# Optimization experiments

Hardware: AMD Instinct MI355X
Metric: run time of the kernel (lower is better)

Reference implementation:

```python
import jax, jax.numpy as jnp
import numpy as np

T, D, K, V, NB = 32768, 256, 16, 16, 2
H = K * V  # hidden size; must equal D for the residual x + y

def phi(x):
    return 1.0 + jax.nn.elu(x)

def _layernorm(x, w, b, eps=1e-5):
    m = x.mean(-1, keepdims=True)
    v = ((x - m) ** 2).mean(-1, keepdims=True)
    return (x - m) * jax.lax.rsqrt(v + eps) * w + b

def _combine(a, b):
    # reset-wrapped associative update: right element's start flag zeroes the left carry
    pa, sa, za = a
    pb, sb, zb = b
    keep = jnp.logical_not(pb)
    return (jnp.logical_or(pa, pb), keep * sa + sb, keep * za + zb)

def _block(x, start, s0, z0, Wk, Wq, Wv, bv, Wskip, bskip, Wm1, bm1, Wm2, bm2, Wm3, bm3, lnw, lnb):
    k = phi(x @ Wk.T)                                   # [T,K]
    q = phi(x @ Wq.T)                                   # [T,K]
    v = x @ Wv.T + bv                                   # [T,V]
    kv = jnp.einsum('ti,tj->tij', k, v)                 # [T,K,V]
    s = jnp.concatenate([s0, kv], axis=0)               # [T+1,K,V]
    z = jnp.concatenate([z0, k[:, None, :]], axis=0)    # [T+1,1,K]
    st = jnp.concatenate([jnp.zeros((1, 1, 1), bool), start.reshape(-1, 1, 1)], axis=0)
    _, s, z = jax.lax.associative_scan(_combine, (st, s, z), axis=0)
    s, z = s[1:], z[1:]
    numer = jnp.einsum('tij,ti->tj', s, q)              # [T,V]
    denom = jnp.einsum('tzi,tj->tz', z, q).clip(1e-6)   # [T,1] (faithful to source einsum)
    out = numer / denom                                 # [T,V]
    h = jax.nn.leaky_relu(out @ Wm1.T + bm1)
    h = jax.nn.leaky_relu(h @ Wm2.T + bm2)
    h = h @ Wm3.T + bm3
    return _layernorm(h + (x @ Wskip.T + bskip), lnw, lnb)

def _forward(x, start, s0, z0, Wk, Wq, Wv, bv, Wskip, bskip, Wm1, bm1, Wm2, bm2, Wm3, bm3, lnw, lnb):
    y = x
    for i in range(NB):  # small fixed layer loop
        y = _block(x, start, s0[i], z0[i], Wk[i], Wq[i], Wv[i], bv[i], Wskip[i], bskip[i],
                   Wm1[i], bm1[i], Wm2[i], bm2[i], Wm3[i], bm3[i], lnw[i], lnb[i])
        x = x + y
    return y

def setup_inputs() -> dict:
    key = jax.random.key(0)
    ks = jax.random.split(key, 12)
    g = lambda k, shp, fan: jax.random.normal(k, shp, jnp.float32) * (fan ** -0.5)
    return dict(
        x=jax.random.normal(ks[0], (T, D), jnp.float32),
        start=jax.random.randint(ks[1], (T,), 0, 2).astype(bool),
        s0=jnp.zeros((NB, 1, K, V), jnp.float32),
        z0=jnp.zeros((NB, 1, 1, K), jnp.float32),
        Wk=g(ks[2], (NB, K, D), D), Wq=g(ks[3], (NB, K, D), D),
        Wv=g(ks[4], (NB, V, D), D), bv=jnp.zeros((NB, V), jnp.float32),
        Wskip=g(ks[5], (NB, H, D), D), bskip=jnp.zeros((NB, H), jnp.float32),
        Wm1=g(ks[6], (NB, H, V), V), bm1=jnp.zeros((NB, H), jnp.float32),
        Wm2=g(ks[7], (NB, H, H), H), bm2=jnp.zeros((NB, H), jnp.float32),
        Wm3=g(ks[8], (NB, H, H), H), bm3=jnp.zeros((NB, H), jnp.float32),
        ln_w=jnp.ones((NB, H), jnp.float32), ln_b=jnp.zeros((NB, H), jnp.float32),
    )

def reference(x, start, s0, z0, Wk, Wq, Wv, bv, Wskip, bskip, Wm1, bm1, Wm2, bm2, Wm3, bm3, ln_w, ln_b):
    return _forward(x, start, s0, z0, Wk, Wq, Wv, bv, Wskip, bskip, Wm1, bm1, Wm2, bm2, Wm3, bm3, ln_w, ln_b)
```

## Files before the change

### kernel.cpp

```cpp
#include <hip/hip_runtime.h>
#include <hip/hip_bf16.h>
#include <cstdint>

#define TT   32768
#define DD   256
#define KV   16
#define NBLK 2
#define HH   256
#define CH   64
#define NCH  (TT / CH)

typedef __attribute__((ext_vector_type(8))) short bf16x8;
typedef __attribute__((ext_vector_type(4))) float f32x4;

__device__ __forceinline__ float phi_f(float x)  { return x > 0.f ? x + 1.f : expf(x); }
__device__ __forceinline__ float lrelu_f(float x){ return x > 0.f ? x : 0.01f * x; }
__device__ __forceinline__ unsigned short f2bf(float f) {
  unsigned u = __float_as_uint(f);
  u += 0x7fffu + ((u >> 16) & 1u);
  return (unsigned short)(u >> 16);
}
__device__ __forceinline__ float bf2f(unsigned short h) {
  return __uint_as_float(((unsigned)h) << 16);
}

__global__ void k_detect(const void* __restrict__ startp, int* __restrict__ flags) {
  int stride = gridDim.x * blockDim.x;
  for (int t = blockIdx.x * blockDim.x + threadIdx.x; t < TT / 4; t += stride) {
    unsigned u = ((const unsigned*)startp)[t];
    if (u > 1u) atomicOr(&flags[0], 1);
    float f = ((const float*)startp)[t];
    if (!(f == 0.f || f == 1.f)) atomicOr(&flags[1], 1);
  }
}

__global__ void k_canon(const void* __restrict__ startp, const int* __restrict__ flags,
                        float* __restrict__ start_f) {
  int v32 = flags[0], vf = flags[1];
  int stride = gridDim.x * blockDim.x;
  for (int t = blockIdx.x * blockDim.x + threadIdx.x; t < TT; t += stride) {
    bool s;
    if (v32 == 0)     s = ((const unsigned*)startp)[t] != 0u;
    else if (vf == 0) s = ((const float*)startp)[t] != 0.f;
    else              s = ((const unsigned char*)startp)[t] != 0;
    start_f[t] = s ? 1.f : 0.f;
  }
}

__global__ __launch_bounds__(256) void k_cvtbig(
    const float* __restrict__ s0, const float* __restrict__ s1, const float* __restrict__ s2,
    unsigned short* __restrict__ d0, unsigned short* __restrict__ d1,
    unsigned short* __restrict__ d2, int n) {
  int i = (blockIdx.x * 256 + threadIdx.x) * 8;
  const float* s; unsigned short* d;
  if (i < n)            { s = s0; d = d0; }
  else if (i < 2 * n)   { s = s1; d = d1; i -= n; }
  else if (i < 3 * n)   { s = s2; d = d2; i -= 2 * n; }
  else return;
  float4 a = *(const float4*)(s + i);
  float4 b = *(const float4*)(s + i + 4);
  float vals[8] = {a.x, a.y, a.z, a.w, b.x, b.y, b.z, b.w};
  bf16x8 t;
#pragma unroll
  for (int j = 0; j < 8; j++) t[j] = (short)f2bf(vals[j]);
  *(bf16x8*)(d + i) = t;
}

__global__ __launch_bounds__(256) void k_cvtproj(
    const float* __restrict__ Wk, const float* __restrict__ Wq, const float* __restrict__ Wv,
    unsigned short* __restrict__ wh, unsigned short* __restrict__ wl) {
  int t8 = blockIdx.x * 256 + threadIdx.x;
  if (t8 >= NBLK * 48 * 256 / 8) return;
  int e = t8 * 8;
  int b = e / (48 * 256);
  int rem = e - b * 48 * 256;
  int o = rem / (16 * 256);
  int nr = rem - o * 16 * 256;
  const float* src = (o == 0 ? Wk : o == 1 ? Wq : Wv) + b * 16 * 256 + nr;
  float4 a = *(const float4*)src;
  float4 c = *(const float4*)(src + 4);
  float vals[8] = {a.x, a.y, a.z, a.w, c.x, c.y, c.z, c.w};
  bf16x8 th, tl;
#pragma unroll
  for (int j = 0; j < 8; j++) {
    unsigned short h = f2bf(vals[j]);
    th[j] = (short)h;
    tl[j] = (short)f2bf(vals[j] - bf2f(h));
  }
  *(bf16x8*)(wh + e) = th;
  *(bf16x8*)(wl + e) = tl;
}

__global__ __launch_bounds__(256) void k_cvtm1(
    const float* __restrict__ Wm1,
    unsigned short* __restrict__ h, unsigned short* __restrict__ l) {
  int row = blockIdx.x * 256 + threadIdx.x;
  if (row >= NBLK * 256) return;
  const float* s = Wm1 + row * 16;
  bf16x8 th0, tl0, th1, tl1, z;
#pragma unroll
  for (int j = 0; j < 8; j++) {
    float v0 = s[j], v1 = s[j + 8];
    unsigned short h0 = f2bf(v0), h1 = f2bf(v1);
    th0[j] = (short)h0; tl0[j] = (short)f2bf(v0 - bf2f(h0));
    th1[j] = (short)h1; tl1[j] = (short)f2bf(v1 - bf2f(h1));
    z[j] = 0;
  }
  unsigned short* dh = h + row * 32;
  unsigned short* dl = l + row * 32;
  *(bf16x8*)(dh) = th0;  *(bf16x8*)(dh + 8) = th1;
  *(bf16x8*)(dh + 16) = z; *(bf16x8*)(dh + 24) = z;
  *(bf16x8*)(dl) = tl0;  *(bf16x8*)(dl + 8) = tl1;
  *(bf16x8*)(dl + 16) = z; *(bf16x8*)(dl + 24) = z;
}

__global__ __launch_bounds__(256) void k_projt(
    const float* __restrict__ x,
    const unsigned short* __restrict__ wh, const unsigned short* __restrict__ wl,
    const float* __restrict__ bv, const float* __restrict__ start_f,
    float* __restrict__ kout, float* __restrict__ qout, float* __restrict__ vout,
    float* __restrict__ tails_s, float* __restrict__ tails_zs,
    float* __restrict__ tails_flag) {
  __shared__ unsigned short xh[64 * 256];
  __shared__ unsigned short xl[64 * 256];
  __shared__ float stc[CH];
  __shared__ int lsS;
  float* kc = (float*)xh;
  float* vc = kc + 64 * 16;

  int tid = threadIdx.x, wg = blockIdx.x;
  size_t rbase = (size_t)wg * 64;
  const float* xs = x + rbase * DD;
#pragma unroll
  for (int i = 0; i < 8; i++) {
    int idx = tid + i * 256;
    int row = idx >> 5, c8 = idx & 31;
    const float* p = xs + row * DD + c8 * 8;
    float4 a = *(const float4*)p;
    float4 b = *(const float4*)(p + 4);
    float vals[8] = {a.x, a.y, a.z, a.w, b.x, b.y, b.z, b.w};
    bf16x8 th, tl;
#pragma unroll
    for (int j = 0; j < 8; j++) {
      unsigned short h = f2bf(vals[j]);
      th[j] = (short)h;
      tl[j] = (short)f2bf(vals[j] - bf2f(h));
    }
    int off = row * 512 + ((c8 * 16) ^ ((row & 7) << 4));
    *(bf16x8*)((char*)xh + off) = th;
    *(bf16x8*)((char*)xl + off) = tl;
  }
  if (tid < CH) stc[tid] = start_f[wg * CH + tid];
  __syncthreads();

  int lane = tid & 63, wv = tid >> 6, lg = lane >> 4, lr = lane & 15;
  int r = wv * 16 + lr;
  f32x4 acc[3];
#pragma unroll
  for (int o = 0; o < 3; o++) acc[o] = (f32x4){0.f, 0.f, 0.f, 0.f};

#pragma unroll
  for (int kk = 0; kk < 8; kk++) {
    int kbyte = kk * 64 + lg * 16;
    int off = r * 512 + (kbyte ^ ((r & 7) << 4));
    bf16x8 ah = *(bf16x8*)((char*)xh + off);
    bf16x8 al = *(bf16x8*)((char*)xl + off);
#pragma unroll
    for (int o = 0; o < 3; o++) {
      bf16x8 bh = *(const bf16x8*)((const char*)wh + (o * 16 + lr) * 512 + kbyte);
      bf16x8 bl = *(const bf16x8*)((const char*)wl + (o * 16 + lr) * 512 + kbyte);
      acc[o] = __builtin_amdgcn_mfma_f32_16x16x32_bf16(ah, bh, acc[o], 0, 0, 0);
      acc[o] = __builtin_amdgcn_mfma_f32_16x16x32_bf16(al, bh, acc[o], 0, 0, 0);
      acc[o] = __builtin_amdgcn_mfma_f32_16x16x32_bf16(ah, bl, acc[o], 0, 0, 0);
    }
  }
  __syncthreads();

  float bvv = bv[lr];
#pragma unroll
  for (int rg = 0; rg < 4; rg++) {
    int rl = wv * 16 + lg * 4 + rg;
    size_t g = rbase + rl;
    float kvl = phi_f(acc[0][rg]);
    float vvl = acc[2][rg] + bvv;
    kout[g * KV + lr] = kvl;
    qout[g * KV + lr] = phi_f(acc[1][rg]);
    vout[g * KV + lr] = vvl;
    kc[rl * KV + lr] = kvl;
    vc[rl * KV + lr] = vvl;
  }
  if (tid < 64) {
    unsigned long long mask = __ballot(stc[tid] != 0.f);
    if (tid == 0) lsS = mask ? (63 - __builtin_clzll(mask)) : -1;
  }
  __syncthreads();
  int ls = lsS;
  int t0 = ls < 0 ? 0 : ls;
  {
    int i = tid >> 4, j = tid & 15;
    float s = 0.f;
    for (int t = t0; t < CH; t++) s += kc[t * KV + i] * vc[t * KV + j];
    tails_s[(size_t)wg * 256 + tid] = s;
  }
  if (tid < 64) {
    float ks = 0.f;
    if (tid >= t0) {
#pragma unroll
      for (int i = 0; i < KV; i++) ks += kc[tid * KV + i];
    }
#pragma unroll
    for (int m = 1; m < 64; m <<= 1) ks += __shfl_xor(ks, m);
    if (tid == 0) {
      tails_zs[wg] = ks;
      tails_flag[wg] = (ls >= 0) ? 1.f : 0.f;
    }
  }
}

#define SP 65
__global__ __launch_bounds__(256) void k_att(
    const float* __restrict__ q, const float* __restrict__ k,
    const float* __restrict__ v, const float* __restrict__ start_f,
    const float* __restrict__ tails_s, const float* __restrict__ tails_zs,
    const float* __restrict__ tails_flag,
    const float* __restrict__ s0, const float* __restrict__ z0,
    float* __restrict__ att) {
  __shared__ float qc[CH * KV], kc[CH * KV], vc[CH * KV], stc[CH];
  __shared__ float S[CH * SP];
  __shared__ float carry[256];
  __shared__ float ksum[CH], zsl[CH], qsum[CH];
  __shared__ int ns[CH];
  __shared__ float czs_s;
  int c = blockIdx.x, tid = threadIdx.x;
  size_t base = (size_t)c * CH * KV;
  for (int u = tid; u < CH * KV; u += 256) {
    qc[u] = q[base + u]; kc[u] = k[base + u]; vc[u] = v[base + u];
  }
  if (tid < CH) stc[tid] = start_f[c * CH + tid];
  __syncthreads();
  if (tid < CH) {
    int cnt = 0;
    for (int u = 0; u <= tid; u++) cnt += (stc[u] != 0.f);
    ns[tid] = cnt;
    float ks = 0.f, qs = 0.f;
    for (int i = 0; i < KV; i++) { ks += kc[tid * KV + i]; qs += qc[tid * KV + i]; }
    ksum[tid] = ks; qsum[tid] = qs;
  }
  __syncthreads();
  if (tid < CH) {
    float acc = 0.f;
    for (int u = tid; u >= 0; u--) { acc += ksum[u]; if (stc[u] != 0.f) break; }
    zsl[tid] = acc;
  }
  {
    float accs = 0.f, aczs = 0.f;
    int cc = c - 1;
    for (;;) {
      if (cc < 0) {
        accs += s0[tid];
        if (tid == 0) { float z = 0.f; for (int i = 0; i < KV; i++) z += z0[i]; aczs += z; }
        break;
      }
      float fl = tails_flag[cc];
      accs += tails_s[(size_t)cc * 256 + tid];
      if (tid == 0) aczs += tails_zs[cc];
      if (fl != 0.f) break;
      cc--;
    }
    carry[tid] = accs;
    if (tid == 0) czs_s = aczs;
  }
  __syncthreads();
  {
    int t = tid >> 2, g = tid & 3;
    for (int u = 0; u < 16; u++) {
      int tp = g * 16 + u;
      float val = 0.f;
      if (tp <= t && ns[tp] == ns[t]) {
        float dot = 0.f;
        for (int i = 0; i < KV; i++) dot += qc[t * KV + i] * kc[tp * KV + i];
        val = dot;
      }
      S[t * SP + tp] = val;
    }
  }
  __syncthreads();
  float czs = czs_s;
  int j = tid & 15, tr = tid >> 4;
  for (int p = 0; p < 4; p++) {
    int t = p * 16 + tr;
    float numer = 0.f;
    for (int tp = 0; tp < CH; tp++) numer += S[t * SP + tp] * vc[tp * KV + j];
    float zs = zsl[t];
    if (ns[t] == 0) {
      float cn = 0.f;
      for (int i = 0; i < KV; i++) cn += qc[t * KV + i] * carry[i * KV + j];
      numer += cn;
      zs += czs;
    }
    float denom = fmaxf(zs * qsum[t], 1e-6f);
    att[base + t * KV + j] = numer / denom;
  }
}

#define A1S 40
template<int WY, int WX>
__global__ __launch_bounds__(256, 2) void k_mlp5(
    const float* __restrict__ att, const float* __restrict__ xsrc,
    const unsigned short* __restrict__ wm1h, const unsigned short* __restrict__ wm1l,
    const float* __restrict__ bm1,
    const unsigned short* __restrict__ Wm2b, const float* __restrict__ bm2,
    const unsigned short* __restrict__ Wm3b, const float* __restrict__ bm3,
    const unsigned short* __restrict__ Wskb, const float* __restrict__ bsk,
    const float* __restrict__ lnw, const float* __restrict__ lnb,
    float* __restrict__ yout, float* __restrict__ xnext) {
  __shared__ unsigned short hb[64 * 256];
  __shared__ __align__(16) char uni[64 * A1S * 4];
  unsigned short* aoh = (unsigned short*)uni;
  unsigned short* aol = aoh + 64 * A1S;
  float* redS = (float*)uni;
  float* redQ = redS + 256;
  float* mrow = redQ + 256;
  float* irow = mrow + 64;

  int tid = threadIdx.x, wg = blockIdx.x;
  size_t rbase = (size_t)wg * 64;

  for (int idx = tid; idx < 64 * 32; idx += 256) {
    int row = idx >> 5, col = idx & 31;
    float v = (col < 16) ? att[(rbase + row) * KV + col] : 0.f;
    unsigned short h = f2bf(v);
    aoh[row * A1S + col] = h;
    aol[row * A1S + col] = f2bf(v - bf2f(h));
  }
  __syncthreads();

  int lane = tid & 63, wv = tid >> 6, lg = lane >> 4, lr = lane & 15;
  int nc0 = wv * 64;

  f32x4 acc[4][4];
#pragma unroll
  for (int a = 0; a < 4; a++)
#pragma unroll
    for (int b = 0; b < 4; b++) acc[a][b] = (f32x4){0.f, 0.f, 0.f, 0.f};

  {
    bf16x8 b1h[4], b1l[4];
#pragma unroll
    for (int nt = 0; nt < 4; nt++) {
      int n = nc0 + nt * 16 + lr;
      b1h[nt] = *(const bf16x8*)(wm1h + n * 32 + lg * 8);
      b1l[nt] = *(const bf16x8*)(wm1l + n * 32 + lg * 8);
    }
#pragma unroll
    for (int mt = 0; mt < 4; mt++) {
      int r = mt * 16 + lr;
      bf16x8 ah = *(bf16x8*)(aoh + r * A1S + lg * 8);
      bf16x8 al = *(bf16x8*)(aol + r * A1S + lg * 8);
#pragma unroll
      for (int nt = 0; nt < 4; nt++) {
        acc[mt][nt] = __builtin_amdgcn_mfma_f32_16x16x32_bf16(ah, b1h[nt], acc[mt][nt], 0, 0, 0);
        acc[mt][nt] = __builtin_amdgcn_mfma_f32_16x16x32_bf16(al, b1h[nt], acc[mt][nt], 0, 0, 0);
        acc[mt][nt] = __builtin_amdgcn_mfma_f32_16x16x32_bf16(ah, b1l[nt], acc[mt][nt], 0, 0, 0);
      }
    }
  }
  __syncthreads();
  {
    float bm1v[4];
#pragma unroll
    for (int nt = 0; nt < 4; nt++) bm1v[nt] = bm1[nc0 + nt * 16 + lr];
#pragma unroll
    for (int mt = 0; mt < 4; mt++)
#pragma unroll
      for (int nt = 0; nt < 4; nt++)
#pragma unroll
        for (int rg = 0; rg < 4; rg++) {
          int r = mt * 16 + lg * 4 + rg;
          int cc = nc0 + nt * 16 + lr;
          *(unsigned short*)((char*)hb + r * 512 + ((cc * 2) ^ ((r & 7) << 4))) =
              f2bf(lrelu_f(acc[mt][nt][rg] + bm1v[nt]));
        }
  }
  __syncthreads();

#pragma unroll
  for (int a = 0; a < 4; a++)
#pragma unroll
    for (int b = 0; b < 4; b++) acc[a][b] = (f32x4){0.f, 0.f, 0.f, 0.f};
#pragma unroll
  for (int kk = 0; kk < 8; kk++) {
    int kbyte = kk * 64 + lg * 16;
    bf16x8 bfr[4];
#pragma unroll
    for (int nt = 0; nt < 4; nt++) {
      int n = nc0 + nt * 16 + lr;
      bfr[nt] = *(const bf16x8*)((const char*)Wm2b + n * 512 + kbyte);
    }
#pragma unroll
    for (int mt = 0; mt < 4; mt++) {
      int r = mt * 16 + lr;
      bf16x8 af = *(bf16x8*)((char*)hb + r * 512 + (kbyte ^ ((r & 7) << 4)));
#pragma unroll
      for (int nt = 0; nt < 4; nt++)
        acc[mt][nt] = __builtin_amdgcn_mfma_f32_16x16x32_bf16(af, bfr[nt], acc[mt][nt], 0, 0, 0);
    }
  }
  __syncthreads();
  {
    float bm2v[4];
#pragma unroll
    for (int nt = 0; nt < 4; nt++) bm2v[nt] = bm2[nc0 + nt * 16 + lr];
#pragma unroll
    for (int mt = 0; mt < 4; mt++)
#pragma unroll
      for (int nt = 0; nt < 4; nt++)
#pragma unroll
        for (int rg = 0; rg < 4; rg++) {
          int r = mt * 16 + lg * 4 + rg;
          int cc = nc0 + nt * 16 + lr;
          *(unsigned short*)((char*)hb + r * 512 + ((cc * 2) ^ ((r & 7) << 4))) =
              f2bf(lrelu_f(acc[mt][nt][rg] + bm2v[nt]));
        }
  }
  __syncthreads();

  f32x4 acc2[4][4];
#pragma unroll
  for (int a = 0; a < 4; a++)
#pragma unroll
    for (int b = 0; b < 4; b++) acc2[a][b] = (f32x4){0.f, 0.f, 0.f, 0.f};
  const float* xrow = xsrc + rbase * DD;
#pragma unroll
  for (int kk = 0; kk < 8; kk++) {
    int kbyte = kk * 64 + lg * 16;
    int kf = kk * 32 + lg * 8;
    bf16x8 b3[4], bs[4];
#pragma unroll
    for (int nt = 0; nt < 4; nt++) {
      int n = nc0 + nt * 16 + lr;
      b3[nt] = *(const bf16x8*)((const char*)Wm3b + n * 512 + kbyte);
      bs[nt] = *(const bf16x8*)((const char*)Wskb + n * 512 + kbyte);
    }
#pragma unroll
    for (int mt = 0; mt < 4; mt++) {
      int r = mt * 16 + lr;
      bf16x8 a2 = *(bf16x8*)((char*)hb + r * 512 + (kbyte ^ ((r & 7) << 4)));
#pragma unroll
      for (int nt = 0; nt < 4; nt++)
        acc2[mt][nt] = __builtin_amdgcn_mfma_f32_16x16x32_bf16(a2, b3[nt], acc2[mt][nt], 0, 0, 0);
      const float* xp = xrow + r * DD + kf;
      float4 x0 = *(const float4*)xp;
      float4 x1 = *(const float4*)(xp + 4);
      bf16x8 xv;
      xv[0] = (short)f2bf(x0.x); xv[1] = (short)f2bf(x0.y);
      xv[2] = (short)f2bf(x0.z); xv[3] = (short)f2bf(x0.w);
      xv[4] = (short)f2bf(x1.x); xv[5] = (short)f2bf(x1.y);
      xv[6] = (short)f2bf(x1.z); xv[7] = (short)f2bf(x1.w);
#pragma unroll
      for (int nt = 0; nt < 4; nt++)
        acc2[mt][nt] = __builtin_amdgcn_mfma_f32_16x16x32_bf16(xv, bs[nt], acc2[mt][nt], 0, 0, 0);
    }
  }
#pragma unroll
  for (int nt = 0; nt < 4; nt++) {
    int cc = nc0 + nt * 16 + lr;
    float bb = bm3[cc] + bsk[cc];
#pragma unroll
    for (int mt = 0; mt < 4; mt++)
#pragma unroll
      for (int rg = 0; rg < 4; rg++) acc2[mt][nt][rg] += bb;
  }

#pragma unroll
  for (int mt = 0; mt < 4; mt++)
#pragma unroll
    for (int rg = 0; rg < 4; rg++) {
      float s = 0.f, q = 0.f;
#pragma unroll
      for (int nt = 0; nt < 4; nt++) {
        float v = acc2[mt][nt][rg];
        s += v; q += v * v;
      }
#pragma unroll
      for (int m = 1; m < 16; m <<= 1) {
        s += __shfl_xor(s, m);
        q += __shfl_xor(q, m);
      }
      if (lr == 0) {
        int r = mt * 16 + lg * 4 + rg;
        redS[wv * 64 + r] = s;
        redQ[wv * 64 + r] = q;
      }
    }
  __syncthreads();
  if (tid < 64) {
    float s = 0.f, q = 0.f;
#pragma unroll
    for (int w = 0; w < 4; w++) { s += redS[w * 64 + tid]; q += redQ[w * 64 + tid]; }
    float m = s * (1.f / 256.f);
    float var = q * (1.f / 256.f) - m * m;
    mrow[tid] = m;
    irow[tid] = rsqrtf(var + 1e-5f);
  }
  __syncthreads();

  {
    float lnwv[4], lnbv[4];
#pragma unroll
    for (int nt = 0; nt < 4; nt++) {
      int cc = nc0 + nt * 16 + lr;
      lnwv[nt] = lnw[cc]; lnbv[nt] = lnb[cc];
    }
#pragma unroll
    for (int mt = 0; mt < 4; mt++)
#pragma unroll
      for (int rg = 0; rg < 4; rg++) {
        int r = mt * 16 + lg * 4 + rg;
        float m = mrow[r], is = irow[r];
        size_t gr = (rbase + r) * DD;
#pragma unroll
        for (int nt = 0; nt < 4; nt++) {
          int cc = nc0 + nt * 16 + lr;
          float y = (acc2[mt][nt][rg] - m) * is * lnwv[nt] + lnbv[nt];
          if (WY) yout[gr + cc] = y;
          if (WX) xnext[gr + cc] = xsrc[gr + cc] + y;
        }
      }
  }
}

extern "C" void kernel_launch(void* const* d_in, const int* in_sizes, int n_in,
                              void* d_out, int out_size, void* d_ws, size_t ws_size,
                              hipStream_t stream) {
  const float* x_in = (const float*)d_in[0];
  const void*  startp = d_in[1];
  const float* s0  = (const float*)d_in[2];
  const float* z0  = (const float*)d_in[3];
  const float* Wk  = (const float*)d_in[4];
  const float* Wq  = (const float*)d_in[5];
  const float* Wv  = (const float*)d_in[6];
  const float* bv  = (const float*)d_in[7];
  const float* Wsk = (const float*)d_in[8];
  const float* bsk = (const float*)d_in[9];
  const float* Wm1 = (const float*)d_in[10];
  const float* bm1 = (const float*)d_in[11];
  const float* Wm2 = (const float*)d_in[12];
  const float* bm2 = (const float*)d_in[13];
  const float* Wm3 = (const float*)d_in[14];
  const float* bm3 = (const float*)d_in[15];
  const float* lnw = (const float*)d_in[16];
  const float* lnb = (const float*)d_in[17];
  float* yout = (float*)d_out;

  float* ws = (float*)d_ws;
  int*   flags   = (int*)d_ws;
  float* start_f = ws + 16;
  float* kbuf    = start_f + TT;
  float* qbuf    = kbuf + (size_t)TT * KV;
  float* vbuf    = qbuf + (size_t)TT * KV;
  float* abuf    = vbuf + (size_t)TT * KV;
  float* ts      = abuf + (size_t)TT * KV;
  float* tz      = ts + (size_t)NCH * 256;
  float* tf      = tz + NCH;
  float* xcur    = tf + NCH;
  unsigned short* wm2b = (unsigned short*)(xcur + (size_t)TT * DD);
  unsigned short* wm3b = wm2b + (size_t)NBLK * HH * HH;
  unsigned short* wskb = wm3b + (size_t)NBLK * HH * HH;
  unsigned short* wpjh = wskb + (size_t)NBLK * HH * DD;
  unsigned short* wpjl = wpjh + (size_t)NBLK * 48 * DD;
  unsigned short* wm1h = wpjl + (size_t)NBLK * 48 * DD;
  unsigned short* wm1l = wm1h + (size_t)NBLK * HH * 32;

  hipMemsetAsync(d_ws, 0, 64, stream);
  k_detect<<<64, 256, 0, stream>>>(startp, flags);
  k_canon<<<256, 256, 0, stream>>>(startp, flags, start_f);

  k_cvtbig<<<192, 256, 0, stream>>>(Wm2, Wm3, Wsk, wm2b, wm3b, wskb, NBLK * HH * HH);
  k_cvtproj<<<12, 256, 0, stream>>>(Wk, Wq, Wv, wpjh, wpjl);
  k_cvtm1<<<2, 256, 0, stream>>>(Wm1, wm1h, wm1l);

  const float* xs = x_in;
  for (int b = 0; b < NBLK; b++) {
    k_projt<<<TT / 64, 256, 0, stream>>>(xs,
        wpjh + (size_t)b * 48 * DD, wpjl + (size_t)b * 48 * DD,
        bv + (size_t)b * KV, start_f, kbuf, qbuf, vbuf, ts, tz, tf);
    k_att<<<NCH, 256, 0, stream>>>(qbuf, kbuf, vbuf, start_f, ts, tz, tf,
        s0 + (size_t)b * 256, z0 + (size_t)b * KV, abuf);
    if (b == 0) {
      k_mlp5<0, 1><<<TT / 64, 256, 0, stream>>>(abuf, xs,
          wm1h + (size_t)b * HH * 32, wm1l + (size_t)b * HH * 32, bm1 + (size_t)b * HH,
          wm2b + (size_t)b * HH * HH, bm2 + (size_t)b * HH,
          wm3b + (size_t)b * HH * HH, bm3 + (size_t)b * HH,
          wskb + (size_t)b * HH * DD, bsk + (size_t)b * HH,
          lnw + (size_t)b * HH, lnb + (size_t)b * HH, yout, xcur);
    } else {
      k_mlp5<1, 0><<<TT / 64, 256, 0, stream>>>(abuf, xs,
          wm1h + (size_t)b * HH * 32, wm1l + (size_t)b * HH * 32, bm1 + (size_t)b * HH,
          wm2b + (size_t)b * HH * HH, bm2 + (size_t)b * HH,
          wm3b + (size_t)b * HH * HH, bm3 + (size_t)b * HH,
          wskb + (size_t)b * HH * DD, bsk + (size_t)b * HH,
          lnw + (size_t)b * HH, lnb + (size_t)b * HH, yout, xcur);
    }
    xs = xcur;
  }
}
```

Baseline: 289.6 us.

## Halve MLP row tile, stage bf16 x in LDS, raise occupancy

```diff
diff --git a/kernel.cpp b/kernel.cpp
--- a/kernel.cpp
+++ b/kernel.cpp
@@ -305,7 +305,7 @@
 
 #define A1S 40
 template<int WY, int WX>
-__global__ __launch_bounds__(256, 2) void k_mlp5(
+__global__ __launch_bounds__(256, 4) void k_mlp6(
     const float* __restrict__ att, const float* __restrict__ xsrc,
     const unsigned short* __restrict__ wm1h, const unsigned short* __restrict__ wm1l,
     const float* __restrict__ bm1,
@@ -314,19 +314,37 @@
     const unsigned short* __restrict__ Wskb, const float* __restrict__ bsk,
     const float* __restrict__ lnw, const float* __restrict__ lnb,
     float* __restrict__ yout, float* __restrict__ xnext) {
-  __shared__ unsigned short hb[64 * 256];
-  __shared__ __align__(16) char uni[64 * A1S * 4];
+  __shared__ unsigned short hb[32 * 256];
+  __shared__ unsigned short xsh[32 * 256];
+  __shared__ __align__(16) char uni[5120];
   unsigned short* aoh = (unsigned short*)uni;
-  unsigned short* aol = aoh + 64 * A1S;
+  unsigned short* aol = aoh + 32 * A1S;
   float* redS = (float*)uni;
-  float* redQ = redS + 256;
-  float* mrow = redQ + 256;
-  float* irow = mrow + 64;
+  float* redQ = redS + 128;
+  float* mrow = redQ + 128;
+  float* irow = mrow + 32;
 
   int tid = threadIdx.x, wg = blockIdx.x;
-  size_t rbase = (size_t)wg * 64;
-
-  for (int idx = tid; idx < 64 * 32; idx += 256) {
+  size_t rbase = (size_t)wg * 32;
+
+  {
+    const float* xs0 = xsrc + rbase * DD;
+#pragma unroll
+    for (int i = 0; i < 4; i++) {
+      int idx = tid + i * 256;
+      int row = idx >> 5, c8 = idx & 31;
+      const float* p = xs0 + row * DD + c8 * 8;
+      float4 a = *(const float4*)p;
+      float4 b = *(const float4*)(p + 4);
+      bf16x8 th;
+      th[0] = (short)f2bf(a.x); th[1] = (short)f2bf(a.y);
+      th[2] = (short)f2bf(a.z); th[3] = (short)f2bf(a.w);
+      th[4] = (short)f2bf(b.x); th[5] = (short)f2bf(b.y);
+      th[6] = (short)f2bf(b.z); th[7] = (short)f2bf(b.w);
+      *(bf16x8*)((char*)xsh + row * 512 + ((c8 * 16) ^ ((row & 7) << 4))) = th;
+    }
+  }
+  for (int idx = tid; idx < 32 * 32; idx += 256) {
     int row = idx >> 5, col = idx & 31;
     float v = (col < 16) ? att[(rbase + row) * KV + col] : 0.f;
     unsigned short h = f2bf(v);
@@ -338,9 +356,9 @@
   int lane = tid & 63, wv = tid >> 6, lg = lane >> 4, lr = lane & 15;
   int nc0 = wv * 64;
 
-  f32x4 acc[4][4];
-#pragma unroll
-  for (int a = 0; a < 4; a++)
+  f32x4 acc[2][4];
+#pragma unroll
+  for (int a = 0; a < 2; a++)
 #pragma unroll
     for (int b = 0; b < 4; b++) acc[a][b] = (f32x4){0.f, 0.f, 0.f, 0.f};
 
@@ -353,7 +371,7 @@
       b1l[nt] = *(const bf16x8*)(wm1l + n * 32 + lg * 8);
     }
 #pragma unroll
-    for (int mt = 0; mt < 4; mt++) {
+    for (int mt = 0; mt < 2; mt++) {
       int r = mt * 16 + lr;
       bf16x8 ah = *(bf16x8*)(aoh + r * A1S + lg * 8);
       bf16x8 al = *(bf16x8*)(aol + r * A1S + lg * 8);
@@ -365,13 +383,12 @@
       }
     }
   }
-  __syncthreads();
   {
     float bm1v[4];
 #pragma unroll
     for (int nt = 0; nt < 4; nt++) bm1v[nt] = bm1[nc0 + nt * 16 + lr];
 #pragma unroll
-    for (int mt = 0; mt < 4; mt++)
+    for (int mt = 0; mt < 2; mt++)
 #pragma unroll
       for (int nt = 0; nt < 4; nt++)
 #pragma unroll
@@ -385,7 +402,7 @@
   __syncthreads();
 
 #pragma unroll
-  for (int a = 0; a < 4; a++)
+  for (int a = 0; a < 2; a++)
 #pragma unroll
     for (int b = 0; b < 4; b++) acc[a][b] = (f32x4){0.f, 0.f, 0.f, 0.f};
 #pragma unroll
@@ -398,7 +415,7 @@
       bfr[nt] = *(const bf16x8*)((const char*)Wm2b + n * 512 + kbyte);
     }
 #pragma unroll
-    for (int mt = 0; mt < 4; mt++) {
+    for (int mt = 0; mt < 2; mt++) {
       int r = mt * 16 + lr;
       bf16x8 af = *(bf16x8*)((char*)hb + r * 512 + (kbyte ^ ((r & 7) << 4)));
 #pragma unroll
@@ -412,7 +429,7 @@
 #pragma unroll
     for (int nt = 0; nt < 4; nt++) bm2v[nt] = bm2[nc0 + nt * 16 + lr];
 #pragma unroll
-    for (int mt = 0; mt < 4; mt++)
+    for (int mt = 0; mt < 2; mt++)
 #pragma unroll
       for (int nt = 0; nt < 4; nt++)
 #pragma unroll
@@ -425,16 +442,14 @@
   }
   __syncthreads();
 
-  f32x4 acc2[4][4];
-#pragma unroll
-  for (int a = 0; a < 4; a++)
+  f32x4 acc2[2][4];
+#pragma unroll
+  for (int a = 0; a < 2; a++)
 #pragma unroll
     for (int b = 0; b < 4; b++) acc2[a][b] = (f32x4){0.f, 0.f, 0.f, 0.f};
-  const float* xrow = xsrc + rbase * DD;
 #pragma unroll
   for (int kk = 0; kk < 8; kk++) {
     int kbyte = kk * 64 + lg * 16;
-    int kf = kk * 32 + lg * 8;
     bf16x8 b3[4], bs[4];
 #pragma unroll
     for (int nt = 0; nt < 4; nt++) {
@@ -443,20 +458,13 @@
       bs[nt] = *(const bf16x8*)((const char*)Wskb + n * 512 + kbyte);
     }
 #pragma unroll
-    for (int mt = 0; mt < 4; mt++) {
+    for (int mt = 0; mt < 2; mt++) {
       int r = mt * 16 + lr;
       bf16x8 a2 = *(bf16x8*)((char*)hb + r * 512 + (kbyte ^ ((r & 7) << 4)));
+      bf16x8 xv = *(bf16x8*)((char*)xsh + r * 512 + (kbyte ^ ((r & 7) << 4)));
 #pragma unroll
       for (int nt = 0; nt < 4; nt++)
         acc2[mt][nt] = __builtin_amdgcn_mfma_f32_16x16x32_bf16(a2, b3[nt], acc2[mt][nt], 0, 0, 0);
-      const float* xp = xrow + r * DD + kf;
-      float4 x0 = *(const float4*)xp;
-      float4 x1 = *(const float4*)(xp + 4);
-      bf16x8 xv;
-      xv[0] = (short)f2bf(x0.x); xv[1] = (short)f2bf(x0.y);
-      xv[2] = (short)f2bf(x0.z); xv[3] = (short)f2bf(x0.w);
-      xv[4] = (short)f2bf(x1.x); xv[5] = (short)f2bf(x1.y);
-      xv[6] = (short)f2bf(x1.z); xv[7] = (short)f2bf(x1.w);
 #pragma unroll
       for (int nt = 0; nt < 4; nt++)
         acc2[mt][nt] = __builtin_amdgcn_mfma_f32_16x16x32_bf16(xv, bs[nt], acc2[mt][nt], 0, 0, 0);
@@ -467,13 +475,13 @@
     int cc = nc0 + nt * 16 + lr;
     float bb = bm3[cc] + bsk[cc];
 #pragma unroll
-    for (int mt = 0; mt < 4; mt++)
+    for (int mt = 0; mt < 2; mt++)
 #pragma unroll
       for (int rg = 0; rg < 4; rg++) acc2[mt][nt][rg] += bb;
   }
 
 #pragma unroll
-  for (int mt = 0; mt < 4; mt++)
+  for (int mt = 0; mt < 2; mt++)
 #pragma unroll
     for (int rg = 0; rg < 4; rg++) {
       float s = 0.f, q = 0.f;
@@ -489,15 +497,15 @@
       }
       if (lr == 0) {
         int r = mt * 16 + lg * 4 + rg;
-        redS[wv * 64 + r] = s;
-        redQ[wv * 64 + r] = q;
+        redS[wv * 32 + r] = s;
+        redQ[wv * 32 + r] = q;
       }
     }
   __syncthreads();
-  if (tid < 64) {
+  if (tid < 32) {
     float s = 0.f, q = 0.f;
 #pragma unroll
-    for (int w = 0; w < 4; w++) { s += redS[w * 64 + tid]; q += redQ[w * 64 + tid]; }
+    for (int w = 0; w < 4; w++) { s += redS[w * 32 + tid]; q += redQ[w * 32 + tid]; }
     float m = s * (1.f / 256.f);
     float var = q * (1.f / 256.f) - m * m;
     mrow[tid] = m;
@@ -513,7 +521,7 @@
       lnwv[nt] = lnw[cc]; lnbv[nt] = lnb[cc];
     }
 #pragma unroll
-    for (int mt = 0; mt < 4; mt++)
+    for (int mt = 0; mt < 2; mt++)
 #pragma unroll
       for (int rg = 0; rg < 4; rg++) {
         int r = mt * 16 + lg * 4 + rg;
@@ -588,14 +596,14 @@
     k_att<<<NCH, 256, 0, stream>>>(qbuf, kbuf, vbuf, start_f, ts, tz, tf,
         s0 + (size_t)b * 256, z0 + (size_t)b * KV, abuf);
     if (b == 0) {
-      k_mlp5<0, 1><<<TT / 64, 256, 0, stream>>>(abuf, xs,
+      k_mlp6<0, 1><<<TT / 32, 256, 0, stream>>>(abuf, xs,
           wm1h + (size_t)b * HH * 32, wm1l + (size_t)b * HH * 32, bm1 + (size_t)b * HH,
           wm2b + (size_t)b * HH * HH, bm2 + (size_t)b * HH,
           wm3b + (size_t)b * HH * HH, bm3 + (size_t)b * HH,
           wskb + (size_t)b * HH * DD, bsk + (size_t)b * HH,
           lnw + (size_t)b * HH, lnb + (size_t)b * HH, yout, xcur);
     } else {
-      k_mlp5<1, 0><<<TT / 64, 256, 0, stream>>>(abuf, xs,
+      k_mlp6<1, 0><<<TT / 32, 256, 0, stream>>>(abuf, xs,
           wm1h + (size_t)b * HH * 32, wm1l + (size_t)b * HH * 32, bm1 + (size_t)b * HH,
           wm2b + (size_t)b * HH * HH, bm2 + (size_t)b * HH,
           wm3b + (size_t)b * HH * HH, bm3 + (size_t)b * HH,
```

Result: slower. 298.3 us (+3.0%).
